# Kernel tuning notes

Hardware: AMD Instinct MI355X
Metric: run time of the kernel (lower is better)

The kernel has to match this reference:

```python
import jax, jax.numpy as jnp
import numpy as np

B, D, K, M1, M2 = 256, 128, 32, 64, 32   # batch, n_nodes, K copies, dims[1], dims[2]
H1, H2, L = 128, 64, 32                   # pivae_dims


def setup_inputs() -> dict:
    key = jax.random.key(0)
    ks = iter(jax.random.split(key, 32))

    def rn(shape, scale):
        return jax.random.normal(next(ks), shape, dtype=jnp.float32) * scale

    x = jax.random.normal(next(ks), (B, D), dtype=jnp.float32)

    # per-node fc1 weights: [D, M1, D]; bounds force nonneg with zero diag column
    W1_pos = jnp.abs(rn((D, M1, D), 1.0 / np.sqrt(D)))
    W1_neg = jnp.abs(rn((D, M1, D), 1.0 / np.sqrt(D)))
    eye = jnp.eye(D, dtype=jnp.float32)[:, None, :]   # zero out W[j,:,j]
    W1_pos = W1_pos * (1.0 - eye)
    W1_neg = W1_neg * (1.0 - eye)
    b1_pos = rn((D, M1), 0.02)
    b1_neg = rn((D, M1), 0.02)

    # LocallyConnected stacks: weight [K, m_in, m_out]
    lc1_w = rn((K, M1, M2), 1.0 / np.sqrt(M1)); lc1_b = rn((K, M2), 0.02)
    lc2_w = rn((K, M2, 1), 1.0 / np.sqrt(M2));  lc2_b = rn((K, 1), 0.02)

    # per-sample beta Linear(k,1): weights [B, K], bias [B]
    beta_w = rn((B, K), 1.0 / np.sqrt(K)); beta_b = rn((B,), 0.02)

    # VAE params (encoder -> mu/logvar -> decoder), stored as (in,out) matrices
    enc1_w = rn((K, H1), 1.0 / np.sqrt(K));  enc1_b = jnp.zeros((H1,), jnp.float32)
    enc2_w = rn((H1, H2), 1.0 / np.sqrt(H1)); enc2_b = jnp.zeros((H2,), jnp.float32)
    mu_w = rn((H2, L), 1.0 / np.sqrt(H2));    mu_b = jnp.zeros((L,), jnp.float32)
    lv_w = rn((H2, L), 1.0 / np.sqrt(H2));    lv_b = jnp.zeros((L,), jnp.float32)
    dec1_w = rn((L, H2), 1.0 / np.sqrt(L));   dec1_b = jnp.zeros((H2,), jnp.float32)
    dec2_w = rn((H2, H1), 1.0 / np.sqrt(H2)); dec2_b = jnp.zeros((H1,), jnp.float32)
    dec3_w = rn((H1, K), 1.0 / np.sqrt(H1));  dec3_b = jnp.zeros((K,), jnp.float32)

    eps = jax.random.normal(next(ks), (B, L), dtype=jnp.float32)  # reparam noise

    return dict(x=x, W1_pos=W1_pos, W1_neg=W1_neg, b1_pos=b1_pos, b1_neg=b1_neg,
                lc1_w=lc1_w, lc1_b=lc1_b, lc2_w=lc2_w, lc2_b=lc2_b,
                beta_w=beta_w, beta_b=beta_b,
                enc1_w=enc1_w, enc1_b=enc1_b, enc2_w=enc2_w, enc2_b=enc2_b,
                mu_w=mu_w, mu_b=mu_b, lv_w=lv_w, lv_b=lv_b,
                dec1_w=dec1_w, dec1_b=dec1_b, dec2_w=dec2_w, dec2_b=dec2_b,
                dec3_w=dec3_w, dec3_b=dec3_b, eps=eps)


def reference(x, W1_pos, W1_neg, b1_pos, b1_neg, lc1_w, lc1_b, lc2_w, lc2_b,
              beta_w, beta_b, enc1_w, enc1_b, enc2_w, enc2_b, mu_w, mu_b,
              lv_w, lv_b, dec1_w, dec1_b, dec2_w, dec2_b, dec3_w, dec3_b, eps):
    b, d = x.shape
    k = lc1_w.shape[0]

    # fused per-node fc1: (pos - neg) applied to x with column j zeroed, all j at once
    W1 = W1_pos - W1_neg                      # [D, M1, D]
    b1 = b1_pos - b1_neg                      # [D, M1]
    full = jnp.einsum('bi,jhi->bjh', x, W1)   # as if no column were zeroed
    diagW = jnp.einsum('jhj->jh', W1)         # [D, M1] column-j weight of node j
    phi = full - x[:, :, None] * diagW[None] + b1[None]   # [B, D, M1]

    # expand to K copies, run sigmoid + LocallyConnected stack
    h = jnp.broadcast_to(phi[:, :, None, :], (b, d, k, phi.shape[-1]))
    h = jnp.einsum('bdkm,kmn->bdkn', jax.nn.sigmoid(h), lc1_w) + lc1_b   # [B,D,K,M2]
    h = jnp.einsum('bdkm,kmn->bdkn', jax.nn.sigmoid(h), lc2_w) + lc2_b   # [B,D,K,1]
    last_phi_x = h[..., 0]                    # [B, D, K]

    # per-sample beta projection (batched over B)
    y1 = jnp.einsum('bdk,bk->bd', last_phi_x, beta_w) + beta_b[:, None]

    # VAE on the stacked beta weights [B, K]
    e = jax.nn.relu(beta_w @ enc1_w + enc1_b)
    e = jax.nn.relu(e @ enc2_w + enc2_b)
    mu = e @ mu_w + mu_b
    logvar = e @ lv_w + lv_b
    z = mu + eps * jnp.exp(0.5 * logvar)
    dh = jax.nn.relu(z @ dec1_w + dec1_b)
    dh = jax.nn.relu(dh @ dec2_w + dec2_b)
    recon = dh @ dec3_w + dec3_b              # [B, K]

    y2 = jnp.einsum('bdk,bk->bd', last_phi_x, recon) + beta_b[:, None]
    return (y1, y2, mu, logvar)
```

## Files before the change

kernel.cpp:

```cpp
#include <hip/hip_runtime.h>
#include <stdint.h>

#define BB 256
#define DD 128
#define KK 32
#define MM1 64
#define MM2 32

typedef __attribute__((ext_vector_type(8))) short bf16x8;
typedef __attribute__((ext_vector_type(4))) float f32x4;

#define LOG2E 1.44269504088896f


__device__ __forceinline__ short f2b(float f) {
  uint32_t u = __builtin_bit_cast(uint32_t, f);
  u += 0x7FFFu + ((u >> 16) & 1u);
  return (short)(u >> 16);
}
__device__ __forceinline__ float sigm_pre(float acc, float cpre) {
  return __builtin_amdgcn_rcpf(
      1.0f + __builtin_amdgcn_exp2f(fmaf(acc, -LOG2E, cpre)));
}

__global__ __launch_bounds__(256) void combo_kernel(
    const float* __restrict__ x, const float* __restrict__ W1p,
    const float* __restrict__ W1n, const float* __restrict__ b1p,
    const float* __restrict__ b1n, const float* __restrict__ lc1w,
    const float* __restrict__ lc1b, const float* __restrict__ lc2b,
    const float* __restrict__ betaw,
    const float* __restrict__ enc1w, const float* __restrict__ enc1b,
    const float* __restrict__ enc2w, const float* __restrict__ enc2b,
    const float* __restrict__ muw,  const float* __restrict__ mub,
    const float* __restrict__ lvw,  const float* __restrict__ lvb,
    const float* __restrict__ dec1w, const float* __restrict__ dec1b,
    const float* __restrict__ dec2w, const float* __restrict__ dec2b,
    const float* __restrict__ dec3w, const float* __restrict__ dec3b,
    const float* __restrict__ eps,
    char* __restrict__ ws, float* __restrict__ mu_out,
    float* __restrict__ lv_out)
{
  const int bx = blockIdx.x;
  if (bx < 1024) {
    const int tid = bx * 256 + threadIdx.x;
    {
      float4 a = ((const float4*)W1p)[tid];
      float4 b = ((const float4*)W1n)[tid];
      short4 s;
      s.x = f2b(a.x - b.x); s.y = f2b(a.y - b.y);
      s.z = f2b(a.z - b.z); s.w = f2b(a.w - b.w);
      ((short4*)(ws + 303104))[tid] = s;
    }
    if (tid < 8192) {
      float4 v = ((const float4*)x)[tid];
      short4 s;
      s.x = f2b(v.x); s.y = f2b(v.y); s.z = f2b(v.z); s.w = f2b(v.w);
      ((short4*)(ws + 65536))[tid] = s;
    }
    if (tid < 65536) {
      int k = tid >> 11, n = (tid >> 6) & 31, m = tid & 63;
      ((short*)(ws + 131072))[tid] = f2b(lc1w[k * 2048 + m * 32 + n]);
    }
    if (tid < 8192) {
      ((float*)(ws + 32768))[tid] = betaw[(tid & 255) * 32 + (tid >> 8)];
    }
    if (tid < 1024) { ((float*)(ws + 262144))[tid] = -lc1b[tid] * LOG2E; }
    if (tid < 32) { ((float*)(ws + 266240))[tid] = 0.25f * lc2b[tid]; }
    if (tid < 8192) {
      ((float*)(ws + 270336))[tid] = -(b1p[tid] - b1n[tid]) * LOG2E;
    }
    return;
  }

  const int b = bx - 1024, t = threadIdx.x;
  float* reconT = (float*)ws;
  __shared__ float bw[KK], e1[128], e2[64], zz[32], d1s[64], d2s[128];
  if (t < KK) bw[t] = betaw[b * KK + t];
  __syncthreads();
  if (t < 128) {
    float a0 = enc1b[t], a1 = 0.f;
    #pragma unroll
    for (int k = 0; k < KK; k += 2) {
      a0 = fmaf(bw[k], enc1w[k * 128 + t], a0);
      a1 = fmaf(bw[k + 1], enc1w[(k + 1) * 128 + t], a1);
    }
    e1[t] = fmaxf(a0 + a1, 0.f);
  }
  __syncthreads();
  if (t < 64) {
    float a0 = enc2b[t], a1 = 0.f, a2 = 0.f, a3 = 0.f;
    #pragma unroll 8
    for (int h = 0; h < 128; h += 4) {
      a0 = fmaf(e1[h], enc2w[h * 64 + t], a0);
      a1 = fmaf(e1[h + 1], enc2w[(h + 1) * 64 + t], a1);
      a2 = fmaf(e1[h + 2], enc2w[(h + 2) * 64 + t], a2);
      a3 = fmaf(e1[h + 3], enc2w[(h + 3) * 64 + t], a3);
    }
    e2[t] = fmaxf((a0 + a1) + (a2 + a3), 0.f);
  }
  __syncthreads();
  if (t < 32) {
    float m0 = mub[t], m1 = 0.f, l0 = lvb[t], l1 = 0.f;
    #pragma unroll 8
    for (int h = 0; h < 64; h += 2) {
      float ea = e2[h], eb = e2[h + 1];
      m0 = fmaf(ea, muw[h * 32 + t], m0);
      m1 = fmaf(eb, muw[(h + 1) * 32 + t], m1);
      l0 = fmaf(ea, lvw[h * 32 + t], l0);
      l1 = fmaf(eb, lvw[(h + 1) * 32 + t], l1);
    }
    float m = m0 + m1, l = l0 + l1;
    mu_out[b * 32 + t] = m;
    lv_out[b * 32 + t] = l;
    zz[t] = fmaf(eps[b * 32 + t], __expf(0.5f * l), m);
  }
  __syncthreads();
  if (t < 64) {
    float a0 = dec1b[t], a1 = 0.f;
    #pragma unroll
    for (int l = 0; l < 32; l += 2) {
      a0 = fmaf(zz[l], dec1w[l * 64 + t], a0);
      a1 = fmaf(zz[l + 1], dec1w[(l + 1) * 64 + t], a1);
    }
    d1s[t] = fmaxf(a0 + a1, 0.f);
  }
  __syncthreads();
  if (t < 128) {
    float a0 = dec2b[t], a1 = 0.f, a2 = 0.f, a3 = 0.f;
    #pragma unroll 8
    for (int h = 0; h < 64; h += 4) {
      a0 = fmaf(d1s[h], dec2w[h * 128 + t], a0);
      a1 = fmaf(d1s[h + 1], dec2w[(h + 1) * 128 + t], a1);
      a2 = fmaf(d1s[h + 2], dec2w[(h + 2) * 128 + t], a2);
      a3 = fmaf(d1s[h + 3], dec2w[(h + 3) * 128 + t], a3);
    }
    d2s[t] = fmaxf((a0 + a1) + (a2 + a3), 0.f);
  }
  __syncthreads();
  if (t < 32) {
    float a0 = dec3b[t], a1 = 0.f, a2 = 0.f, a3 = 0.f;
    #pragma unroll 8
    for (int h = 0; h < 128; h += 4) {
      a0 = fmaf(d2s[h], dec3w[h * 32 + t], a0);
      a1 = fmaf(d2s[h + 1], dec3w[(h + 1) * 32 + t], a1);
      a2 = fmaf(d2s[h + 2], dec3w[(h + 2) * 32 + t], a2);
      a3 = fmaf(d2s[h + 3], dec3w[(h + 3) * 32 + t], a3);
    }
    reconT[t * BB + b] = (a0 + a1) + (a2 + a3);
  }
}

__global__ __launch_bounds__(512) void main_kernel(
    const float* __restrict__ lc2w, const float* __restrict__ betab,
    const char* __restrict__ ws, float* __restrict__ out)
{
  const int bx = blockIdx.x;
  const int dp = bx >> 2;
  const int bq = bx & 3;
  const int d0 = dp * 2, d1 = d0 + 1;
  const int tid = threadIdx.x;
  const int wv = tid >> 6, lane = tid & 63;
  const int g = lane >> 4, l15 = lane & 15;

  const short* __restrict__ xbf   = (const short*)(ws + 65536);
  const short* __restrict__ lc1T  = (const short*)(ws + 131072);
  const float* __restrict__ lc1bs = (const float*)(ws + 262144);
  const float* __restrict__ lc2bq = (const float*)(ws + 266240);
  const float* __restrict__ b1s   = (const float*)(ws + 270336);
  const short* __restrict__ w1bf  = (const short*)(ws + 303104);
  const float* __restrict__ betaT = (const float*)(ws + 32768);
  const float* __restrict__ recT  = (const float*)(ws + 0);

  __shared__ __align__(16) short sS[2][64 * 64];
  __shared__ __align__(16) float betaS[KK * 64];
  __shared__ __align__(16) float reconS[KK * 64];
  __shared__ __align__(16) float cS[KK * MM2];
  __shared__ __align__(16) float wSS[KK * MM2];
  __shared__ float lbq[KK];
  __shared__ float yred[8][64][4];

  {
    const int k = tid >> 4, j = (tid & 15) * 4;
    *(float4*)&betaS[k * 64 + j]  = *(const float4*)&betaT[k * BB + bq * 64 + j];
    *(float4*)&reconS[k * 64 + j] = *(const float4*)&recT[k * BB + bq * 64 + j];
  }
  if (tid < 256)      ((f32x4*)cS)[tid]        = ((const f32x4*)lc1bs)[tid];
  else if (tid < 512) ((f32x4*)wSS)[tid - 256] = ((const f32x4*)lc2w)[tid - 256];
  if (tid < KK) lbq[tid] = lc2bq[tid];

  bf16x8 Af[4][2][2];
  #pragma unroll
  for (int kk = 0; kk < 4; ++kk) {
    const short* ap = lc1T + ((wv * 4 + kk) * 32 + l15) * 64 + g * 8;
    Af[kk][0][0] = *(const bf16x8*)(ap);
    Af[kk][0][1] = *(const bf16x8*)(ap + 32);
    Af[kk][1][0] = *(const bf16x8*)(ap + 16 * 64);
    Af[kk][1][1] = *(const bf16x8*)(ap + 16 * 64 + 32);
  }
  const int bt = wv >> 1, mtp = (wv & 1) * 2;
  bf16x8 xa[4];
  {
    const short* xrow = xbf + (bq * 64 + bt * 16 + l15) * DD + g * 8;
    #pragma unroll
    for (int ks = 0; ks < 4; ++ks)
      xa[ks] = *(const bf16x8*)(xrow + ks * 32);
  }

#define PHASE1(dd, which) { \
    const short* wrow = w1bf + (dd) * (MM1 * DD); \
    _Pragma("unroll") \
    for (int mi = 0; mi < 2; ++mi) { \
      const int m = (mtp + mi) * 16 + l15; \
      f32x4 acc = {0.f, 0.f, 0.f, 0.f}; \
      _Pragma("unroll") \
      for (int ks = 0; ks < 4; ++ks) { \
        bf16x8 wb = *(const bf16x8*)(wrow + m * DD + ks * 32 + g * 8); \
        acc = __builtin_amdgcn_mfma_f32_16x16x32_bf16(xa[ks], wb, acc, 0, 0, 0); \
      } \
      const float cpre = b1s[(dd) * MM1 + m]; \
      _Pragma("unroll") \
      for (int r = 0; r < 4; ++r) { \
        const int bl = bt * 16 + g * 4 + r; \
        sS[which][bl * 64 + ((m & ~7) ^ ((bl & 7) << 3)) + (m & 7)] = \
            f2b(sigm_pre(acc[r], cpre)); \
      } \
    } }

#define PHASE2(which, yoff) { \
    bf16x8 sa[4][2]; \
    _Pragma("unroll") \
    for (int rt = 0; rt < 4; ++rt) { \
      const int b = rt * 16 + l15; \
      const int bsw = (b & 7) << 3; \
      sa[rt][0] = *(const bf16x8*)&sS[which][b * 64 + ((g * 8) ^ bsw)]; \
      sa[rt][1] = *(const bf16x8*)&sS[which][b * 64 + ((32 + g * 8) ^ bsw)]; \
    } \
    float y1p[4] = {0, 0, 0, 0}, y2p[4] = {0, 0, 0, 0}; \
    _Pragma("unroll") \
    for (int kk = 0; kk < 4; ++kk) { \
      const int k = wv * 4 + kk; \
      const f32x4 c40 = *(const f32x4*)&cS[k * 32 + g * 4]; \
      const f32x4 c41 = *(const f32x4*)&cS[k * 32 + 16 + g * 4]; \
      const f32x4 w40 = *(const f32x4*)&wSS[k * 32 + g * 4]; \
      const f32x4 w41 = *(const f32x4*)&wSS[k * 32 + 16 + g * 4]; \
      const float lb = lbq[k]; \
      _Pragma("unroll") \
      for (int rt = 0; rt < 4; ++rt) { \
        f32x4 a0 = {0.f, 0.f, 0.f, 0.f}, a1 = {0.f, 0.f, 0.f, 0.f}; \
        a0 = __builtin_amdgcn_mfma_f32_16x16x32_bf16(Af[kk][0][0], sa[rt][0], a0, 0, 0, 0); \
        a0 = __builtin_amdgcn_mfma_f32_16x16x32_bf16(Af[kk][0][1], sa[rt][1], a0, 0, 0, 0); \
        a1 = __builtin_amdgcn_mfma_f32_16x16x32_bf16(Af[kk][1][0], sa[rt][0], a1, 0, 0, 0); \
        a1 = __builtin_amdgcn_mfma_f32_16x16x32_bf16(Af[kk][1][1], sa[rt][1], a1, 0, 0, 0); \
        float v = lb; \
        _Pragma("unroll") \
        for (int r = 0; r < 4; ++r) { \
          v = fmaf(sigm_pre(a0[r], c40[r]), w40[r], v); \
          v = fmaf(sigm_pre(a1[r], c41[r]), w41[r], v); \
        } \
        y1p[rt] = fmaf(v, betaS[k * 64 + rt * 16 + l15], y1p[rt]); \
        y2p[rt] = fmaf(v, reconS[k * 64 + rt * 16 + l15], y2p[rt]); \
      } \
    } \
    _Pragma("unroll") \
    for (int rt = 0; rt < 4; ++rt) { \
      y1p[rt] += __shfl_xor(y1p[rt], 16, 64); \
      y1p[rt] += __shfl_xor(y1p[rt], 32, 64); \
      y2p[rt] += __shfl_xor(y2p[rt], 16, 64); \
      y2p[rt] += __shfl_xor(y2p[rt], 32, 64); \
    } \
    if (g == 0) { \
      _Pragma("unroll") \
      for (int rt = 0; rt < 4; ++rt) { \
        yred[wv][rt * 16 + l15][(yoff)]     = y1p[rt]; \
        yred[wv][rt * 16 + l15][(yoff) + 1] = y2p[rt]; \
      } \
    } }

  PHASE1(d0, 0);
  __syncthreads();
  PHASE1(d1, 1);
  PHASE2(0, 0);
  __syncthreads();
  PHASE2(1, 2);
  __syncthreads();

#undef PHASE1
#undef PHASE2

  if (tid < 256) {
    const int ds = tid >> 7, q = tid & 127, bl = q >> 1, o = q & 1;
    float s = 0.f;
    #pragma unroll
    for (int w = 0; w < 8; ++w) s += yred[w][bl][ds * 2 + o];
    const int b = bq * 64 + bl;
    out[o * (BB * DD) + b * DD + d0 + ds] = s + betab[b];
  }
}

extern "C" void kernel_launch(void* const* d_in, const int* in_sizes, int n_in,
                              void* d_out, int out_size, void* d_ws, size_t ws_size,
                              hipStream_t stream) {
  const float* x     = (const float*)d_in[0];
  const float* W1p   = (const float*)d_in[1];
  const float* W1n   = (const float*)d_in[2];
  const float* b1p   = (const float*)d_in[3];
  const float* b1n   = (const float*)d_in[4];
  const float* lc1w  = (const float*)d_in[5];
  const float* lc1b  = (const float*)d_in[6];
  const float* lc2w  = (const float*)d_in[7];
  const float* lc2b  = (const float*)d_in[8];
  const float* betaw = (const float*)d_in[9];
  const float* betab = (const float*)d_in[10];
  const float* enc1w = (const float*)d_in[11];
  const float* enc1b = (const float*)d_in[12];
  const float* enc2w = (const float*)d_in[13];
  const float* enc2b = (const float*)d_in[14];
  const float* muw   = (const float*)d_in[15];
  const float* mub   = (const float*)d_in[16];
  const float* lvw   = (const float*)d_in[17];
  const float* lvb   = (const float*)d_in[18];
  const float* dec1w = (const float*)d_in[19];
  const float* dec1b = (const float*)d_in[20];
  const float* dec2w = (const float*)d_in[21];
  const float* dec2b = (const float*)d_in[22];
  const float* dec3w = (const float*)d_in[23];
  const float* dec3b = (const float*)d_in[24];
  const float* eps   = (const float*)d_in[25];

  float* out    = (float*)d_out;
  char*  ws     = (char*)d_ws;
  float* mu_out = out + BB * DD * 2;
  float* lv_out = mu_out + BB * 32;

  combo_kernel<<<dim3(1280), dim3(256), 0, stream>>>(
      x, W1p, W1n, b1p, b1n, lc1w, lc1b, lc2b, betaw,
      enc1w, enc1b, enc2w, enc2b, muw, mub, lvw, lvb,
      dec1w, dec1b, dec2w, dec2b, dec3w, dec3b, eps,
      ws, mu_out, lv_out);

  main_kernel<<<dim3(256), dim3(512), 0, stream>>>(
      lc2w, betab, (const char*)ws, out);
}
```

Baseline: 139.5 us.

## Fuse W1 and x bf16 conversion into main kernel via LDS staging

```diff
diff --git a/kernel.cpp b/kernel.cpp
--- a/kernel.cpp
+++ b/kernel.cpp
@@ -23,12 +23,8 @@
       1.0f + __builtin_amdgcn_exp2f(fmaf(acc, -LOG2E, cpre)));
 }
 
-__global__ __launch_bounds__(256) void combo_kernel(
-    const float* __restrict__ x, const float* __restrict__ W1p,
-    const float* __restrict__ W1n, const float* __restrict__ b1p,
-    const float* __restrict__ b1n, const float* __restrict__ lc1w,
-    const float* __restrict__ lc1b, const float* __restrict__ lc2b,
-    const float* __restrict__ betaw,
+__global__ __launch_bounds__(256) void pre_kernel(
+    const float* __restrict__ betaw, const float* __restrict__ lc1w,
     const float* __restrict__ enc1w, const float* __restrict__ enc1b,
     const float* __restrict__ enc2w, const float* __restrict__ enc2b,
     const float* __restrict__ muw,  const float* __restrict__ mub,
@@ -41,38 +37,14 @@
     float* __restrict__ lv_out)
 {
   const int bx = blockIdx.x;
-  if (bx < 1024) {
-    const int tid = bx * 256 + threadIdx.x;
-    {
-      float4 a = ((const float4*)W1p)[tid];
-      float4 b = ((const float4*)W1n)[tid];
-      short4 s;
-      s.x = f2b(a.x - b.x); s.y = f2b(a.y - b.y);
-      s.z = f2b(a.z - b.z); s.w = f2b(a.w - b.w);
-      ((short4*)(ws + 303104))[tid] = s;
-    }
-    if (tid < 8192) {
-      float4 v = ((const float4*)x)[tid];
-      short4 s;
-      s.x = f2b(v.x); s.y = f2b(v.y); s.z = f2b(v.z); s.w = f2b(v.w);
-      ((short4*)(ws + 65536))[tid] = s;
-    }
-    if (tid < 65536) {
-      int k = tid >> 11, n = (tid >> 6) & 31, m = tid & 63;
-      ((short*)(ws + 131072))[tid] = f2b(lc1w[k * 2048 + m * 32 + n]);
-    }
-    if (tid < 8192) {
-      ((float*)(ws + 32768))[tid] = betaw[(tid & 255) * 32 + (tid >> 8)];
-    }
-    if (tid < 1024) { ((float*)(ws + 262144))[tid] = -lc1b[tid] * LOG2E; }
-    if (tid < 32) { ((float*)(ws + 266240))[tid] = 0.25f * lc2b[tid]; }
-    if (tid < 8192) {
-      ((float*)(ws + 270336))[tid] = -(b1p[tid] - b1n[tid]) * LOG2E;
-    }
+  if (bx >= 256) {
+    const int e = (bx - 256) * 256 + threadIdx.x;
+    const int k = e >> 11, n = (e >> 6) & 31, m = e & 63;
+    ((short*)(ws + 32768))[e] = f2b(lc1w[k * 2048 + m * 32 + n]);
     return;
   }
 
-  const int b = bx - 1024, t = threadIdx.x;
+  const int b = bx, t = threadIdx.x;
   float* reconT = (float*)ws;
   __shared__ float bw[KK], e1[128], e2[64], zz[32], d1s[64], d2s[128];
   if (t < KK) bw[t] = betaw[b * KK + t];
@@ -151,42 +123,73 @@
 }
 
 __global__ __launch_bounds__(512) void main_kernel(
-    const float* __restrict__ lc2w, const float* __restrict__ betab,
+    const float* __restrict__ x,
+    const float* __restrict__ W1p, const float* __restrict__ W1n,
+    const float* __restrict__ b1p, const float* __restrict__ b1n,
+    const float* __restrict__ lc1b, const float* __restrict__ lc2w,
+    const float* __restrict__ lc2b, const float* __restrict__ betaw,
+    const float* __restrict__ betab,
     const char* __restrict__ ws, float* __restrict__ out)
 {
   const int bx = blockIdx.x;
   const int dp = bx >> 2;
   const int bq = bx & 3;
-  const int d0 = dp * 2, d1 = d0 + 1;
+  const int d0 = dp * 2;
   const int tid = threadIdx.x;
   const int wv = tid >> 6, lane = tid & 63;
   const int g = lane >> 4, l15 = lane & 15;
 
-  const short* __restrict__ xbf   = (const short*)(ws + 65536);
-  const short* __restrict__ lc1T  = (const short*)(ws + 131072);
-  const float* __restrict__ lc1bs = (const float*)(ws + 262144);
-  const float* __restrict__ lc2bq = (const float*)(ws + 266240);
-  const float* __restrict__ b1s   = (const float*)(ws + 270336);
-  const short* __restrict__ w1bf  = (const short*)(ws + 303104);
-  const float* __restrict__ betaT = (const float*)(ws + 32768);
-  const float* __restrict__ recT  = (const float*)(ws + 0);
-
+  const short* __restrict__ lc1T = (const short*)(ws + 32768);
+  const float* __restrict__ recT = (const float*)(ws + 0);
+
+  __shared__ __align__(16) short w1S[2][64 * 128];
   __shared__ __align__(16) short sS[2][64 * 64];
   __shared__ __align__(16) float betaS[KK * 64];
   __shared__ __align__(16) float reconS[KK * 64];
   __shared__ __align__(16) float cS[KK * MM2];
   __shared__ __align__(16) float wSS[KK * MM2];
   __shared__ float lbq[KK];
+  __shared__ float b1sS[2][MM1];
   __shared__ float yred[8][64][4];
 
+  #pragma unroll
+  for (int ds = 0; ds < 2; ++ds) {
+    const float* wp = W1p + (d0 + ds) * (MM1 * DD);
+    const float* wn = W1n + (d0 + ds) * (MM1 * DD);
+    #pragma unroll
+    for (int e = tid; e < 2048; e += 512) {
+      const int m = e >> 5, c = (e & 31) * 4;
+      float4 a = *(const float4*)(wp + m * 128 + c);
+      float4 b = *(const float4*)(wn + m * 128 + c);
+      short4 s;
+      s.x = f2b(a.x - b.x); s.y = f2b(a.y - b.y);
+      s.z = f2b(a.z - b.z); s.w = f2b(a.w - b.w);
+      *(short4*)&w1S[ds][m * 128 + ((c & ~7) ^ ((m & 7) << 3)) + (c & 7)] = s;
+    }
+  }
   {
     const int k = tid >> 4, j = (tid & 15) * 4;
-    *(float4*)&betaS[k * 64 + j]  = *(const float4*)&betaT[k * BB + bq * 64 + j];
-    *(float4*)&reconS[k * 64 + j] = *(const float4*)&recT[k * BB + bq * 64 + j];
-  }
-  if (tid < 256)      ((f32x4*)cS)[tid]        = ((const f32x4*)lc1bs)[tid];
-  else if (tid < 512) ((f32x4*)wSS)[tid - 256] = ((const f32x4*)lc2w)[tid - 256];
-  if (tid < KK) lbq[tid] = lc2bq[tid];
+    const float* bwp = betaw + (bq * 64 + j) * 32 + k;
+    betaS[k * 64 + j]     = bwp[0];
+    betaS[k * 64 + j + 1] = bwp[32];
+    betaS[k * 64 + j + 2] = bwp[64];
+    betaS[k * 64 + j + 3] = bwp[96];
+    *(float4*)&reconS[k * 64 + j] =
+        *(const float4*)&recT[k * BB + bq * 64 + j];
+  }
+  if (tid < 256) {
+    f32x4 v = ((const f32x4*)lc1b)[tid];
+    f32x4 o = {-v[0] * LOG2E, -v[1] * LOG2E, -v[2] * LOG2E, -v[3] * LOG2E};
+    ((f32x4*)cS)[tid] = o;
+  } else if (tid < 512) {
+    ((f32x4*)wSS)[tid - 256] = ((const f32x4*)lc2w)[tid - 256];
+  }
+  if (tid < KK) lbq[tid] = 0.25f * lc2b[tid];
+  if (tid < 128) {
+    const int ds = tid >> 6, mm = tid & 63;
+    b1sS[ds][mm] =
+        -(b1p[(d0 + ds) * MM1 + mm] - b1n[(d0 + ds) * MM1 + mm]) * LOG2E;
+  }
 
   bf16x8 Af[4][2][2];
   #pragma unroll
@@ -200,24 +203,29 @@
   const int bt = wv >> 1, mtp = (wv & 1) * 2;
   bf16x8 xa[4];
   {
-    const short* xrow = xbf + (bq * 64 + bt * 16 + l15) * DD + g * 8;
-    #pragma unroll
-    for (int ks = 0; ks < 4; ++ks)
-      xa[ks] = *(const bf16x8*)(xrow + ks * 32);
-  }
-
-#define PHASE1(dd, which) { \
-    const short* wrow = w1bf + (dd) * (MM1 * DD); \
+    const float* xrow = x + (bq * 64 + bt * 16 + l15) * DD + g * 8;
+    #pragma unroll
+    for (int ks = 0; ks < 4; ++ks) {
+      float4 lo = *(const float4*)(xrow + ks * 32);
+      float4 hi = *(const float4*)(xrow + ks * 32 + 4);
+      xa[ks] = (bf16x8){f2b(lo.x), f2b(lo.y), f2b(lo.z), f2b(lo.w),
+                        f2b(hi.x), f2b(hi.y), f2b(hi.z), f2b(hi.w)};
+    }
+  }
+  __syncthreads();
+
+#define PHASE1(ds, which) { \
     _Pragma("unroll") \
     for (int mi = 0; mi < 2; ++mi) { \
       const int m = (mtp + mi) * 16 + l15; \
       f32x4 acc = {0.f, 0.f, 0.f, 0.f}; \
       _Pragma("unroll") \
       for (int ks = 0; ks < 4; ++ks) { \
-        bf16x8 wb = *(const bf16x8*)(wrow + m * DD + ks * 32 + g * 8); \
+        const int c0 = ks * 32 + g * 8; \
+        bf16x8 wb = *(const bf16x8*)&w1S[ds][m * 128 + (c0 ^ ((m & 7) << 3))]; \
         acc = __builtin_amdgcn_mfma_f32_16x16x32_bf16(xa[ks], wb, acc, 0, 0, 0); \
       } \
-      const float cpre = b1s[(dd) * MM1 + m]; \
+      const float cpre = b1sS[ds][m]; \
       _Pragma("unroll") \
       for (int r = 0; r < 4; ++r) { \
         const int bl = bt * 16 + g * 4 + r; \
@@ -276,9 +284,9 @@
       } \
     } }
 
-  PHASE1(d0, 0);
-  __syncthreads();
-  PHASE1(d1, 1);
+  PHASE1(0, 0);
+  __syncthreads();
+  PHASE1(1, 1);
   PHASE2(0, 0);
   __syncthreads();
   PHASE2(1, 2);
@@ -332,12 +340,12 @@
   float* mu_out = out + BB * DD * 2;
   float* lv_out = mu_out + BB * 32;
 
-  combo_kernel<<<dim3(1280), dim3(256), 0, stream>>>(
-      x, W1p, W1n, b1p, b1n, lc1w, lc1b, lc2b, betaw,
-      enc1w, enc1b, enc2w, enc2b, muw, mub, lvw, lvb,
+  pre_kernel<<<dim3(512), dim3(256), 0, stream>>>(
+      betaw, lc1w, enc1w, enc1b, enc2w, enc2b, muw, mub, lvw, lvb,
       dec1w, dec1b, dec2w, dec2b, dec3w, dec3b, eps,
       ws, mu_out, lv_out);
 
   main_kernel<<<dim3(256), dim3(512), 0, stream>>>(
-      lc2w, betab, (const char*)ws, out);
-}
+      x, W1p, W1n, b1p, b1n, lc1b, lc2w, lc2b, betaw, betab,
+      (const char*)ws, out);
+}
```

After: 139.0 us. No clear change (-0.4%).
